# Performance work log

Hardware: AMD Instinct MI355X
Metric: run time of the kernel (lower is better)

## Reference

```python
import jax, jax.numpy as jnp
import numpy as np

N_CONTEXT = 9
N_INPUT = 26
WINDOW = 2 * N_CONTEXT + 1  # 19
BATCH, TIME = 64, 2000


def setup_inputs() -> dict:
    key = jax.random.key(0)
    x = jax.random.normal(key, (BATCH, TIME, N_INPUT), dtype=jnp.float32)
    return {"x": x}


def reference(x):
    # The original uses conv1d with an identity filter of shape
    # (window, channels, window*channels) and SAME padding. That is exactly
    # a zero-padded sliding-window unfold: output[b, t] = flatten of
    # x[b, t-n_context : t+n_context+1, :] (zero padded at edges).
    B, T, C = x.shape
    xp = jnp.pad(x, ((0, 0), (N_CONTEXT, N_CONTEXT), (0, 0)))  # [B, T+2*ctx, C]
    # gather indices for each output position: [T, WINDOW]
    idx = jnp.arange(T)[:, None] + jnp.arange(WINDOW)[None, :]
    win = xp[:, idx, :]  # [B, T, WINDOW, C]
    return win.reshape(-1, WINDOW * C)  # [B*T, WINDOW*C]
```

## Files before the change

kernel.cpp:

```cpp
#include <hip/hip_runtime.h>

constexpr int N_CONTEXT = 9;
constexpr int C        = 26;
constexpr int WINDOW   = 2 * N_CONTEXT + 1;
constexpr int BATCH    = 64;
constexpr int TIME     = 2000;
constexpr int ROW      = WINDOW * C;
constexpr int ROW2     = ROW / 2;

__global__ __launch_bounds__(256)
void CreateOverlappingWindows_84963043050043_kernel(const float* __restrict__ x,
                                                    float* __restrict__ out) {
    const int p = blockIdx.x * blockDim.x + threadIdx.x;

    const int r  = p / ROW2;
    const int j2 = p - r * ROW2;
    const int j  = j2 * 2;

    const int t = r % TIME;
    const int w = j / C;
    const int src_t = t + w - N_CONTEXT;

    float2 v = make_float2(0.0f, 0.0f);
    if ((unsigned)src_t < (unsigned)TIME) {
        const int off = (r - N_CONTEXT) * C + j;
        v = *reinterpret_cast<const float2*>(x + off);
    }
    reinterpret_cast<float2*>(out)[p] = v;
}

extern "C" void kernel_launch(void* const* d_in, const int* in_sizes, int n_in,
                              void* d_out, int out_size, void* d_ws, size_t ws_size,
                              hipStream_t stream) {
    const float* x = (const float*)d_in[0];
    float* out = (float*)d_out;

    constexpr long long total_pairs = (long long)BATCH * TIME * ROW2;
    constexpr int block = 256;
    constexpr int grid  = (int)(total_pairs / block);

    CreateOverlappingWindows_84963043050043_kernel<<<grid, block, 0, stream>>>(x, out);
}
```

Before: 297.9 us.

## Stage time tile in LDS and emit float4 nontemporal output stores

Each block loads a 16-timestep tile plus halo of the input into shared memory, zero-padding at batch edges. It then writes the unfolded windows with 128-bit nontemporal stores instead of per-thread 64-bit loads and stores from global memory. The aim is to cut redundant global reads and raise store width and efficiency for this write-bound kernel. The cost is a block barrier and LDS indexing, including special handling for vectors that straddle output rows.

```diff
diff --git a/kernel.cpp b/kernel.cpp
--- a/kernel.cpp
+++ b/kernel.cpp
@@ -1,32 +1,63 @@
 #include <hip/hip_runtime.h>
 
 constexpr int N_CONTEXT = 9;
-constexpr int C        = 26;
-constexpr int WINDOW   = 2 * N_CONTEXT + 1;
-constexpr int BATCH    = 64;
-constexpr int TIME     = 2000;
-constexpr int ROW      = WINDOW * C;
-constexpr int ROW2     = ROW / 2;
+constexpr int C         = 26;
+constexpr int WINDOW    = 2 * N_CONTEXT + 1;
+constexpr int BATCH     = 64;
+constexpr int TIME      = 2000;
+constexpr int ROW       = WINDOW * C;
 
-__global__ __launch_bounds__(256)
+constexpr int T_TILE      = 16;
+constexpr int LDS_ROWS    = T_TILE + WINDOW - 1;
+constexpr int LDS_FLOATS  = LDS_ROWS * C;
+constexpr int TILE_FLOATS = T_TILE * ROW;
+constexpr int TILE_VEC4   = TILE_FLOATS / 4;
+constexpr int BLOCK       = 256;
+constexpr int NBLOCKS     = BATCH * TIME / T_TILE;
+constexpr int BATCH_FLOATS = TIME * C;
+
+typedef float vfloat4 __attribute__((ext_vector_type(4)));
+
+__global__ __launch_bounds__(BLOCK)
 void CreateOverlappingWindows_84963043050043_kernel(const float* __restrict__ x,
                                                     float* __restrict__ out) {
-    const int p = blockIdx.x * blockDim.x + threadIdx.x;
+    __shared__ float lds[LDS_FLOATS];
+    const int blk = blockIdx.x;
+    const int tid = threadIdx.x;
+    const int r0  = blk * T_TILE;
+    const int b   = r0 / TIME;
+    const int lo  = b * BATCH_FLOATS;
+    const int hi  = lo + BATCH_FLOATS;
+    const int g0  = (r0 - N_CONTEXT) * C;
 
-    const int r  = p / ROW2;
-    const int j2 = p - r * ROW2;
-    const int j  = j2 * 2;
+    #pragma unroll
+    for (int it = 0; it < (LDS_FLOATS + BLOCK - 1) / BLOCK; ++it) {
+        int idx = tid + it * BLOCK;
+        if (idx < LDS_FLOATS) {
+            int g = g0 + idx;
+            lds[idx] = (g >= lo && g < hi) ? x[g] : 0.0f;
+        }
+    }
+    __syncthreads();
 
-    const int t = r % TIME;
-    const int w = j / C;
-    const int src_t = t + w - N_CONTEXT;
-
-    float2 v = make_float2(0.0f, 0.0f);
-    if ((unsigned)src_t < (unsigned)TIME) {
-        const int off = (r - N_CONTEXT) * C + j;
-        v = *reinterpret_cast<const float2*>(x + off);
+    vfloat4* out4 = reinterpret_cast<vfloat4*>(out) + (size_t)blk * TILE_VEC4;
+    #pragma unroll
+    for (int it = 0; it < (TILE_VEC4 + BLOCK - 1) / BLOCK; ++it) {
+        int q = tid + it * BLOCK;
+        if (q < TILE_VEC4) {
+            int f  = q * 4;
+            int lt = f / ROW;
+            int j  = f - lt * ROW;
+            int a  = lt * C + j;
+            int sub = (j == ROW - 2) ? (ROW - C) : 0;
+            vfloat4 v;
+            v.x = lds[a];
+            v.y = lds[a + 1];
+            v.z = lds[a + 2 - sub];
+            v.w = lds[a + 3 - sub];
+            __builtin_nontemporal_store(v, &out4[q]);
+        }
     }
-    reinterpret_cast<float2*>(out)[p] = v;
 }
 
 extern "C" void kernel_launch(void* const* d_in, const int* in_sizes, int n_in,
@@ -34,10 +65,5 @@
                               hipStream_t stream) {
     const float* x = (const float*)d_in[0];
     float* out = (float*)d_out;
-
-    constexpr long long total_pairs = (long long)BATCH * TIME * ROW2;
-    constexpr int block = 256;
-    constexpr int grid  = (int)(total_pairs / block);
-
-    CreateOverlappingWindows_84963043050043_kernel<<<grid, block, 0, stream>>>(x, out);
+    CreateOverlappingWindows_84963043050043_kernel<<<NBLOCKS, BLOCK, 0, stream>>>(x, out);
 }
```

New measurement: 257.8 us. -13.5%, faster.

## Write 16-byte nontemporal stores with multiple iterations per thread

Applied to the files above, without the earlier changes.

Each thread now writes a float4 of output instead of a float2, handling the case where the four floats span two window slots or two rows. Each thread also processes five strided chunks with incrementally updated indices, which amortises the divide and modulo work. Output stores use nontemporal hints to avoid polluting the cache with the large write-only stream. The price is extra branching for the straddle case and two conditional 8-byte loads per store.

```diff
diff --git a/kernel.cpp b/kernel.cpp
--- a/kernel.cpp
+++ b/kernel.cpp
@@ -1,32 +1,60 @@
 #include <hip/hip_runtime.h>
 
 constexpr int N_CONTEXT = 9;
-constexpr int C        = 26;
-constexpr int WINDOW   = 2 * N_CONTEXT + 1;
-constexpr int BATCH    = 64;
-constexpr int TIME     = 2000;
-constexpr int ROW      = WINDOW * C;
-constexpr int ROW2     = ROW / 2;
+constexpr int C      = 26;
+constexpr int WINDOW = 2 * N_CONTEXT + 1;
+constexpr int BATCH  = 64;
+constexpr int TIME   = 2000;
+constexpr int ROW    = WINDOW * C;
 
-__global__ __launch_bounds__(256)
+constexpr long long OUT_FLOATS = (long long)BATCH * TIME * ROW;
+constexpr int OUT_VEC4   = (int)(OUT_FLOATS / 4);
+constexpr int BLOCK      = 256;
+constexpr int ITERS      = 5;
+constexpr int GRID       = OUT_VEC4 / (BLOCK * ITERS);
+constexpr int STRIDE_V4  = GRID * BLOCK;
+constexpr int R_STEP     = STRIDE_V4 * 4 / ROW;
+constexpr int T_STEP     = R_STEP % TIME;
+constexpr int SRC_STEP   = STRIDE_V4 * 4 - 468 * R_STEP;
+
+typedef float vfloat4 __attribute__((ext_vector_type(4)));
+
+__global__ __launch_bounds__(BLOCK)
 void CreateOverlappingWindows_84963043050043_kernel(const float* __restrict__ x,
                                                     float* __restrict__ out) {
-    const int p = blockIdx.x * blockDim.x + threadIdx.x;
+    const int tid = blockIdx.x * BLOCK + threadIdx.x;
+    const int F   = tid * 4;
+    const int r   = F / ROW;
+    const int j   = F - r * ROW;
+    int       t   = r % TIME;
+    const int w0  = j / C;
+    const int m   = j - w0 * C;
+    const bool straddle = (j == ROW - 2);
+    const int w1   = straddle ? 0 : ((m == C - 2) ? w0 + 1 : w0);
+    const int dt1  = straddle ? 1 : 0;
+    const int off1 = straddle ? (2 - (ROW - C)) : 2;
+    int       src  = F - (ROW - C) * r - N_CONTEXT * C;
 
-    const int r  = p / ROW2;
-    const int j2 = p - r * ROW2;
-    const int j  = j2 * 2;
+    #pragma unroll
+    for (int i = 0; i < ITERS; ++i) {
+        const int st0 = t + w0 - N_CONTEXT;
+        int t1 = t + dt1; if (t1 == TIME) t1 = 0;
+        const int st1 = t1 + w1 - N_CONTEXT;
 
-    const int t = r % TIME;
-    const int w = j / C;
-    const int src_t = t + w - N_CONTEXT;
+        float2 p0 = make_float2(0.0f, 0.0f);
+        float2 p1 = make_float2(0.0f, 0.0f);
+        if ((unsigned)st0 < (unsigned)TIME)
+            p0 = *reinterpret_cast<const float2*>(x + src);
+        if ((unsigned)st1 < (unsigned)TIME)
+            p1 = *reinterpret_cast<const float2*>(x + src + off1);
 
-    float2 v = make_float2(0.0f, 0.0f);
-    if ((unsigned)src_t < (unsigned)TIME) {
-        const int off = (r - N_CONTEXT) * C + j;
-        v = *reinterpret_cast<const float2*>(x + off);
+        vfloat4 v; v.x = p0.x; v.y = p0.y; v.z = p1.x; v.w = p1.y;
+        __builtin_nontemporal_store(
+            v, reinterpret_cast<vfloat4*>(out) + tid + i * STRIDE_V4);
+
+        t += T_STEP; if (t >= TIME) t -= TIME;
+        src += SRC_STEP;
     }
-    reinterpret_cast<float2*>(out)[p] = v;
 }
 
 extern "C" void kernel_launch(void* const* d_in, const int* in_sizes, int n_in,
@@ -34,10 +62,5 @@
                               hipStream_t stream) {
     const float* x = (const float*)d_in[0];
     float* out = (float*)d_out;
-
-    constexpr long long total_pairs = (long long)BATCH * TIME * ROW2;
-    constexpr int block = 256;
-    constexpr int grid  = (int)(total_pairs / block);
-
-    CreateOverlappingWindows_84963043050043_kernel<<<grid, block, 0, stream>>>(x, out);
+    CreateOverlappingWindows_84963043050043_kernel<<<GRID, BLOCK, 0, stream>>>(x, out);
 }
```

New measurement: 280.8 us. 1.06x faster.
